# Kernel tuning notes

Measured on AMD Instinct MI355X. Metric: run time of the kernel, lower is better.

Reference implementation:

```python
import jax, jax.numpy as jnp
import numpy as np

N_NODES = 50000
N_EDGES = 800000
IN_CH, HID_CH, OUT_CH = 128, 128, 64


def setup_inputs() -> dict:
    key = jax.random.key(0)
    ks = jax.random.split(key, 8)
    x = jax.random.normal(ks[0], (N_NODES, IN_CH), dtype=jnp.float32)
    edge_index = jax.random.randint(ks[1], (2, N_EDGES), 0, N_NODES, dtype=jnp.int64)
    # PyG SAGEConv params: lin_l (applied to aggregated neighbors, has bias),
    # lin_r (applied to root node, no bias). Stored here as [in, out] matrices.
    s1 = 1.0 / np.sqrt(IN_CH)
    s2 = 1.0 / np.sqrt(HID_CH)
    W1l = jax.random.uniform(ks[2], (IN_CH, HID_CH), jnp.float32, -s1, s1)
    b1 = jnp.zeros((HID_CH,), jnp.float32)
    W1r = jax.random.uniform(ks[3], (IN_CH, HID_CH), jnp.float32, -s1, s1)
    W2l = jax.random.uniform(ks[4], (HID_CH, OUT_CH), jnp.float32, -s2, s2)
    b2 = jnp.zeros((OUT_CH,), jnp.float32)
    W2r = jax.random.uniform(ks[5], (HID_CH, OUT_CH), jnp.float32, -s2, s2)
    return {"x": x, "edge_index": edge_index, "W1l": W1l, "b1": b1,
            "W1r": W1r, "W2l": W2l, "b2": b2, "W2r": W2r}


def _sage_conv(x, src, dst, Wl, b, Wr):
    # mean-aggregate source features onto targets, then linear transform
    msg = x[src]                                        # [E, d] gather
    agg = jax.ops.segment_sum(msg, dst, num_segments=N_NODES)   # [N, d]
    deg = jax.ops.segment_sum(jnp.ones((src.shape[0],), x.dtype), dst,
                              num_segments=N_NODES)     # [N]
    mean = agg / jnp.maximum(deg, 1.0)[:, None]
    return mean @ Wl + b + x @ Wr


def reference(x, edge_index, W1l, b1, W1r, W2l, b2, W2r):
    src, dst = edge_index[0], edge_index[1]
    h = jax.nn.relu(_sage_conv(x, src, dst, W1l, b1, W1r))
    # F.dropout(p=0.3) is identity in eval mode
    return _sage_conv(h, src, dst, W2l, b2, W2r)
```

## Files before the change

kernel.cpp:

```cpp
#include <hip/hip_runtime.h>
#include <hip/hip_bf16.h>


#define TBLOCK 256
#define MAXBUCK 256
#define HGRID 512

typedef __attribute__((ext_vector_type(8))) short short8;
typedef __attribute__((ext_vector_type(4))) float f32x4;

__device__ __forceinline__ float bf2f(ushort u) {
    union { unsigned int i; float f; } v;
    v.i = (unsigned int)u << 16;
    return v.f;
}
__device__ __forceinline__ ushort f2bf(float f) {
    union { float f; unsigned int u; } v;
    v.f = f;
    unsigned int r = v.u + 0x7fffu + ((v.u >> 16) & 1u);
    return (ushort)(r >> 16);
}

__device__ __forceinline__ int block_detect_is64(const int* __restrict__ edges) {
    __shared__ int sbad[4];
    int tid = threadIdx.x;
    int bad = 0;
    for (int i = tid; i < 2048; i += TBLOCK)
        if (edges[2 * i + 1] != 0) bad = 1;
    unsigned long long b = __ballot(bad);
    if ((tid & 63) == 0) sbad[tid >> 6] = (b != 0) ? 1 : 0;
    __syncthreads();
    int flag = (sbad[0] | sbad[1] | sbad[2] | sbad[3]) ? 0 : 1;
    __syncthreads();
    return flag;
}

__device__ __forceinline__ int load_src(const int* e, long long i, int E, int is64) {
    return is64 ? e[2 * i] : e[i];
}
__device__ __forceinline__ int load_dst(const int* e, long long i, int E, int is64) {
    return is64 ? e[2 * (long long)E + 2 * i] : e[(long long)E + i];
}

__device__ __forceinline__ void scan_total(const int* __restrict__ total, int NBUCK,
                                           int* __restrict__ s) {
    int t = threadIdx.x;
    s[t] = (t < NBUCK) ? total[t] : 0;
    __syncthreads();
    for (int off = 1; off < TBLOCK; off <<= 1) {
        int xv = (t >= off) ? s[t - off] : 0;
        __syncthreads();
        s[t] += xv;
        __syncthreads();
    }
}

__global__ __launch_bounds__(TBLOCK) void histprep_k(
    const float* __restrict__ x,
    const float* __restrict__ W1l, const float* __restrict__ W1r,
    const float* __restrict__ W2l, const float* __restrict__ W2r,
    const int* __restrict__ edges, int E, int NBUCK,
    ushort* __restrict__ xb, ushort* __restrict__ wc1, ushort* __restrict__ wc2,
    int* __restrict__ counts, int n8, int nxb) {
    __shared__ int lh[MAXBUCK];
    const int b = blockIdx.x;
    const int t = threadIdx.x;
    if (b < HGRID) {
        const int is64 = block_detect_is64(edges);
        for (int i = t; i < NBUCK; i += TBLOCK) lh[i] = 0;
        __syncthreads();
        const int per = (E + HGRID - 1) / HGRID;
        const int b0 = b * per, b1 = min(E, b0 + per);
        for (int i = b0 + t; i < b1; i += TBLOCK)
            atomicAdd(&lh[load_dst(edges, i, E, is64) >> 8], 1);
        __syncthreads();
        for (int j = t; j < NBUCK; j += TBLOCK)
            counts[j * HGRID + b] = lh[j];
    } else {
        int pb = b - HGRID;
        if (pb < nxb) {
            int i = pb * TBLOCK + t;
            if (i >= n8) return;
            const float4* p = (const float4*)x + (size_t)i * 2;
            float4 a = p[0], bb = p[1];
            short8 o;
            o[0] = f2bf(a.x); o[1] = f2bf(a.y); o[2] = f2bf(a.z); o[3] = f2bf(a.w);
            o[4] = f2bf(bb.x); o[5] = f2bf(bb.y); o[6] = f2bf(bb.z); o[7] = f2bf(bb.w);
            *(short8*)(xb + (size_t)i * 8) = o;
        } else {
            int i = (pb - nxb) * TBLOCK + t;
            if (i < 32768) {
                int j = i & 7;
                int rest = i >> 3;
                int n = rest & 127;
                int k = ((rest >> 7) << 3) | j;
                float w = (k < 128) ? W1l[k * 128 + n] : W1r[(k - 128) * 128 + n];
                wc1[i] = f2bf(w);
            } else if (i < 49152) {
                int i2 = i - 32768;
                int j = i2 & 7;
                int rest = i2 >> 3;
                int n = rest & 127;
                int k = ((rest >> 7) << 3) | j;
                float w = (n < 64) ? W2l[k * 64 + n] : W2r[k * 64 + (n - 64)];
                wc2[i2] = f2bf(w);
            }
        }
    }
}

__global__ __launch_bounds__(TBLOCK) void scanA_k(int* __restrict__ counts,
                                                  int* __restrict__ total) {
    __shared__ int s[TBLOCK];
    const int j = blockIdx.x;
    const int t = threadIdx.x;
    int* row = counts + (size_t)j * HGRID;
    int v0 = row[2 * t];
    int v1 = row[2 * t + 1];
    s[t] = v0 + v1;
    __syncthreads();
    for (int off = 1; off < TBLOCK; off <<= 1) {
        int xv = (t >= off) ? s[t - off] : 0;
        __syncthreads();
        s[t] += xv;
        __syncthreads();
    }
    int excl = (t == 0) ? 0 : s[t - 1];
    row[2 * t] = excl;
    row[2 * t + 1] = excl + v0;
    if (t == TBLOCK - 1) total[j] = s[t];
}

__global__ __launch_bounds__(TBLOCK) void scatroot_k(
    const int* __restrict__ edges, int E,
    const int* __restrict__ counts, const int* __restrict__ total,
    unsigned int* __restrict__ packed, int NBUCK,
    const ushort* __restrict__ xb, const ushort* __restrict__ wc1,
    const float* __restrict__ b1, ushort* __restrict__ hb, int N, int RB) {
    __shared__ __align__(16) ushort sW[128 * 128];
    __shared__ int s[TBLOCK];
    __shared__ int lb[MAXBUCK];
    __shared__ int lh[MAXBUCK];
    const int t = threadIdx.x;

    if ((int)blockIdx.x < RB) {
        const ushort* wroot = wc1 + 16384;
        for (int i = t * 8; i < 128 * 128; i += TBLOCK * 8)
            *(short8*)&sW[i] = *(const short8*)&wroot[i];
        __syncthreads();
        const int wave = t >> 6;
        const int lane = t & 63;
        const int quad = lane >> 4;
        const int l16 = lane & 15;
        const int m0 = (blockIdx.x * 4 + wave) * 32;
        if (m0 >= N) return;
        f32x4 acc[2][8];
#pragma unroll
        for (int tt = 0; tt < 2; tt++)
#pragma unroll
            for (int nt = 0; nt < 8; nt++) acc[tt][nt] = (f32x4){0.f, 0.f, 0.f, 0.f};
        const int k0q = quad * 8;
#pragma unroll
        for (int kb = 0; kb < 128; kb += 32) {
            int k = kb + k0q;
            short8 a[2];
#pragma unroll
            for (int tt = 0; tt < 2; tt++) {
                int m = m0 + tt * 16 + l16;
                if (m > N - 1) m = N - 1;
                a[tt] = *(const short8*)(xb + (size_t)m * 128 + k);
            }
#pragma unroll
            for (int nt = 0; nt < 8; nt++) {
                short8 b = *(const short8*)&sW[((k >> 3) * 128 + nt * 16 + l16) * 8];
                acc[0][nt] = __builtin_amdgcn_mfma_f32_16x16x32_bf16(a[0], b, acc[0][nt], 0, 0, 0);
                acc[1][nt] = __builtin_amdgcn_mfma_f32_16x16x32_bf16(a[1], b, acc[1][nt], 0, 0, 0);
            }
        }
#pragma unroll
        for (int tt = 0; tt < 2; tt++)
#pragma unroll
            for (int r = 0; r < 4; r++) {
                int m = m0 + tt * 16 + quad * 4 + r;
                if (m >= N) continue;
#pragma unroll
                for (int nt = 0; nt < 8; nt++) {
                    int n = nt * 16 + l16;
                    hb[(size_t)m * 128 + n] = f2bf(acc[tt][nt][r] + b1[n]);
                }
            }
    } else {
        const int b = blockIdx.x - RB;
        const int is64 = block_detect_is64(edges);
        scan_total(total, NBUCK, s);
        if (t < NBUCK) {
            int excl = (t == 0) ? 0 : s[t - 1];
            lb[t] = excl + counts[t * HGRID + b];
            lh[t] = 0;
        }
        __syncthreads();
        const int per = (E + HGRID - 1) / HGRID;
        const int b0 = b * per, b1e = min(E, b0 + per);
        for (int i = b0 + t; i < b1e; i += TBLOCK) {
            int sv = load_src(edges, i, E, is64);
            int d = load_dst(edges, i, E, is64);
            int bk = d >> 8;
            int pos = lb[bk] + atomicAdd(&lh[bk], 1);
            packed[pos] = (unsigned int)sv | ((unsigned int)(d & 255) << 24);
        }
    }
}

__global__ __launch_bounds__(TBLOCK) void buildB_k(const unsigned int* __restrict__ packed,
                                                   const int* __restrict__ total,
                                                   int* __restrict__ offs,
                                                   int* __restrict__ degi,
                                                   float* __restrict__ invdeg,
                                                   int* __restrict__ csr, int N, int NBUCK) {
    __shared__ int s[TBLOCK];
    __shared__ int cnt[TBLOCK], scn[TBLOCK], cur[TBLOCK];
    int t = threadIdx.x;
    int bucket = blockIdx.x;
    scan_total(total, NBUCK, s);
    int e0 = (bucket == 0) ? 0 : s[bucket - 1];
    int e1 = s[bucket];
    cnt[t] = 0;
    cur[t] = 0;
    __syncthreads();
    for (int i = e0 + t; i < e1; i += TBLOCK)
        atomicAdd(&cnt[packed[i] >> 24], 1);
    __syncthreads();
    scn[t] = cnt[t];
    __syncthreads();
    for (int off = 1; off < TBLOCK; off <<= 1) {
        int x = (t >= off) ? scn[t - off] : 0;
        __syncthreads();
        scn[t] += x;
        __syncthreads();
    }
    int excl = (t == 0) ? 0 : scn[t - 1];
    int node = bucket * 256 + t;
    if (node < N) {
        offs[node] = e0 + excl;
        degi[node] = cnt[t];
        invdeg[node] = 1.0f / fmaxf((float)cnt[t], 1.0f);
    }
    __syncthreads();
    cnt[t] = excl;
    __syncthreads();
    for (int i = e0 + t; i < e1; i += TBLOCK) {
        unsigned int p = packed[i];
        int nl = p >> 24;
        int pos = e0 + cnt[nl] + atomicAdd(&cur[nl], 1);
        csr[pos] = (int)(p & 0xFFFFFFu);
    }
}

template <int C, bool ACCUM>
__global__ __launch_bounds__(TBLOCK) void gatherb_k(const ushort* __restrict__ feat,
                                                    const int* __restrict__ csr,
                                                    const int* __restrict__ offs,
                                                    const int* __restrict__ degi,
                                                    const float* __restrict__ invdeg,
                                                    ushort* __restrict__ outB,
                                                    float* __restrict__ outF, int N) {
    constexpr int G = C / 8;
    constexpr int NPB = TBLOCK / G;
    int n = blockIdx.x * NPB + threadIdx.x / G;
    if (n >= N) return;
    int lane = threadIdx.x % G;
    int c = lane * 8;
    int s0 = offs[n];
    int d = degi[n];
    float acc[8] = {0.f, 0.f, 0.f, 0.f, 0.f, 0.f, 0.f, 0.f};
    for (int base = 0; base < d; base += G) {
        int rem = d - base;
        int my = (lane < rem) ? csr[s0 + base + lane] : 0;
        if (rem >= G) {
#pragma unroll
            for (int j = 0; j < G; j++) {
                int s = __shfl(my, j, G);
                short8 v = *(const short8*)(feat + (size_t)s * C + c);
#pragma unroll
                for (int q = 0; q < 8; q++) acc[q] += bf2f((ushort)v[q]);
            }
        } else {
            for (int j = 0; j < rem; j++) {
                int s = __shfl(my, j, G);
                short8 v = *(const short8*)(feat + (size_t)s * C + c);
#pragma unroll
                for (int q = 0; q < 8; q++) acc[q] += bf2f((ushort)v[q]);
            }
        }
    }
    float sc = invdeg[n];
    if (ACCUM) {
        float* o = outF + (size_t)n * C + c;
        float4 p0 = *(float4*)o;
        float4 p1 = *(float4*)(o + 4);
        p0.x += sc * acc[0]; p0.y += sc * acc[1]; p0.z += sc * acc[2]; p0.w += sc * acc[3];
        p1.x += sc * acc[4]; p1.y += sc * acc[5]; p1.z += sc * acc[6]; p1.w += sc * acc[7];
        *(float4*)o = p0;
        *(float4*)(o + 4) = p1;
    } else {
        short8 o;
#pragma unroll
        for (int q = 0; q < 8; q++) o[q] = f2bf(sc * acc[q]);
        *(short8*)(outB + (size_t)n * C + c) = o;
    }
}

__global__ __launch_bounds__(TBLOCK) void gemm1b_k(const ushort* __restrict__ agg1b,
                                                   const ushort* __restrict__ wc1,
                                                   ushort* __restrict__ hb, int N) {
    __shared__ __align__(16) ushort sW[128 * 128];
    for (int i = threadIdx.x * 8; i < 128 * 128; i += TBLOCK * 8)
        *(short8*)&sW[i] = *(const short8*)&wc1[i];
    __syncthreads();

    const int wave = threadIdx.x >> 6;
    const int lane = threadIdx.x & 63;
    const int quad = lane >> 4;
    const int l16 = lane & 15;
    const int m0 = (blockIdx.x * 4 + wave) * 32;
    if (m0 >= N) return;

    f32x4 acc[2][8];
#pragma unroll
    for (int t = 0; t < 2; t++)
#pragma unroll
        for (int nt = 0; nt < 8; nt++) acc[t][nt] = (f32x4){0.f, 0.f, 0.f, 0.f};

    const int k0q = quad * 8;
#pragma unroll
    for (int kb = 0; kb < 128; kb += 32) {
        int k = kb + k0q;
        short8 a[2];
#pragma unroll
        for (int t = 0; t < 2; t++) {
            int m = m0 + t * 16 + l16;
            if (m > N - 1) m = N - 1;
            a[t] = *(const short8*)(agg1b + (size_t)m * 128 + k);
        }
#pragma unroll
        for (int nt = 0; nt < 8; nt++) {
            short8 b = *(const short8*)&sW[((k >> 3) * 128 + nt * 16 + l16) * 8];
            acc[0][nt] = __builtin_amdgcn_mfma_f32_16x16x32_bf16(a[0], b, acc[0][nt], 0, 0, 0);
            acc[1][nt] = __builtin_amdgcn_mfma_f32_16x16x32_bf16(a[1], b, acc[1][nt], 0, 0, 0);
        }
    }

#pragma unroll
    for (int t = 0; t < 2; t++) {
#pragma unroll
        for (int r = 0; r < 4; r++) {
            int m = m0 + t * 16 + quad * 4 + r;
            if (m >= N) continue;
#pragma unroll
            for (int nt = 0; nt < 8; nt++) {
                int n = nt * 16 + l16;
                float v = acc[t][nt][r] + bf2f(hb[(size_t)m * 128 + n]);
                hb[(size_t)m * 128 + n] = f2bf(fmaxf(v, 0.f));
            }
        }
    }
}

__global__ __launch_bounds__(TBLOCK) void gemm2_k(const ushort* __restrict__ A0,
                                                  const ushort* __restrict__ wc,
                                                  const float* __restrict__ bias,
                                                  ushort* __restrict__ outB,
                                                  float* __restrict__ outF, int N) {
    constexpr int KTOT = 128;
    __shared__ __align__(16) ushort sW[KTOT * 128];
    for (int i = threadIdx.x * 8; i < KTOT * 128; i += TBLOCK * 8)
        *(short8*)&sW[i] = *(const short8*)&wc[i];
    __syncthreads();

    const int wave = threadIdx.x >> 6;
    const int lane = threadIdx.x & 63;
    const int quad = lane >> 4;
    const int l16 = lane & 15;
    const int m0 = (blockIdx.x * 4 + wave) * 32;
    if (m0 >= N) return;

    f32x4 acc[2][8];
#pragma unroll
    for (int t = 0; t < 2; t++)
#pragma unroll
        for (int nt = 0; nt < 8; nt++) acc[t][nt] = (f32x4){0.f, 0.f, 0.f, 0.f};

    const int k0q = quad * 8;
#pragma unroll
    for (int kb = 0; kb < KTOT; kb += 32) {
        int k = kb + k0q;
        short8 a[2];
#pragma unroll
        for (int t = 0; t < 2; t++) {
            int m = m0 + t * 16 + l16;
            if (m > N - 1) m = N - 1;
            a[t] = *(const short8*)(A0 + (size_t)m * 128 + k);
        }
#pragma unroll
        for (int nt = 0; nt < 8; nt++) {
            short8 b = *(const short8*)&sW[((k >> 3) * 128 + nt * 16 + l16) * 8];
            acc[0][nt] = __builtin_amdgcn_mfma_f32_16x16x32_bf16(a[0], b, acc[0][nt], 0, 0, 0);
            acc[1][nt] = __builtin_amdgcn_mfma_f32_16x16x32_bf16(a[1], b, acc[1][nt], 0, 0, 0);
        }
    }

#pragma unroll
    for (int t = 0; t < 2; t++) {
#pragma unroll
        for (int r = 0; r < 4; r++) {
            int m = m0 + t * 16 + quad * 4 + r;
            if (m >= N) continue;
#pragma unroll
            for (int nt = 0; nt < 8; nt++) {
                int n = nt * 16 + l16;
                float v = acc[t][nt][r];
                if (n < 64) outB[(size_t)m * 64 + n] = f2bf(v);
                else outF[(size_t)m * 64 + (n - 64)] = v + bias[n - 64];
            }
        }
    }
}

extern "C" void kernel_launch(void* const* d_in, const int* in_sizes, int n_in,
                              void* d_out, int out_size, void* d_ws, size_t ws_size,
                              hipStream_t stream) {
    const float* x = (const float*)d_in[0];
    const int* edges = (const int*)d_in[1];
    const float* W1l = (const float*)d_in[2];
    const float* b1 = (const float*)d_in[3];
    const float* W1r = (const float*)d_in[4];
    const float* W2l = (const float*)d_in[5];
    const float* b2 = (const float*)d_in[6];
    const float* W2r = (const float*)d_in[7];
    float* out = (float*)d_out;

    const int N = in_sizes[0] / 128;
    const int E = in_sizes[1] / 2;
    const int Na = (N + 63) & ~63;
    const int NBUCK = (N + 255) >> 8;
    const int n8 = N * 128 / 8;
    const int nxb = (n8 + TBLOCK - 1) / TBLOCK;
    const int RB = (N + 127) / 128;

    char* WS = (char*)d_ws;
    size_t off = 0;
    auto alloc = [&](size_t bytes) {
        void* p = WS + off;
        off = (off + bytes + 255) & ~(size_t)255;
        return p;
    };
    int* counts = (int*)alloc((size_t)MAXBUCK * HGRID * 4);
    int* total = (int*)alloc((size_t)MAXBUCK * 4);
    int* offs = (int*)alloc((size_t)Na * 4);
    int* degi = (int*)alloc((size_t)Na * 4);
    float* invdeg = (float*)alloc((size_t)Na * 4);
    unsigned int* packed = (unsigned int*)alloc((size_t)E * 4);
    int* csr = (int*)alloc((size_t)E * 4);
    ushort* xb = (ushort*)alloc((size_t)N * 128 * 2);
    ushort* agg1b = (ushort*)alloc((size_t)N * 128 * 2);
    ushort* hb = (ushort*)alloc((size_t)N * 128 * 2);
    ushort* t2b = (ushort*)alloc((size_t)N * 64 * 2);
    ushort* wc1 = (ushort*)alloc(32768 * 2);
    ushort* wc2 = (ushort*)alloc(16384 * 2);

    histprep_k<<<HGRID + nxb + 192, TBLOCK, 0, stream>>>(
        x, W1l, W1r, W2l, W2r, edges, E, NBUCK, xb, wc1, wc2, counts, n8, nxb);
    scanA_k<<<NBUCK, TBLOCK, 0, stream>>>(counts, total);
    scatroot_k<<<RB + HGRID, TBLOCK, 0, stream>>>(
        edges, E, counts, total, packed, NBUCK, xb, wc1, b1, hb, N, RB);
    buildB_k<<<NBUCK, TBLOCK, 0, stream>>>(packed, total, offs, degi, invdeg, csr, N, NBUCK);

    gatherb_k<128, false><<<(N + 15) / 16, TBLOCK, 0, stream>>>(
        xb, csr, offs, degi, invdeg, agg1b, nullptr, N);
    gemm1b_k<<<(N + 127) / 128, TBLOCK, 0, stream>>>(agg1b, wc1, hb, N);

    gemm2_k<<<(N + 127) / 128, TBLOCK, 0, stream>>>(
        hb, wc2, b2, t2b, out, N);
    gatherb_k<64, true><<<(N + 31) / 32, TBLOCK, 0, stream>>>(
        t2b, csr, offs, degi, invdeg, nullptr, out, N);
}
```

Measured before the change: 194.2 us.

## Fuse layer-1 and layer-2 GEMMs, keeping hidden activations in LDS

Merges the two GEMM kernels into one. The ReLU'd hidden tile is staged in padded shared memory, then multiplied by the second weight matrix in the same block. This removes the global write and re-read of the hidden activations and one kernel launch. In exchange, LDS use per block roughly doubles (weights plus the hidden tile), which may lower occupancy, and an extra weight reload and barriers are added.

```diff
diff --git a/kernel.cpp b/kernel.cpp
--- a/kernel.cpp
+++ b/kernel.cpp
@@ -5,6 +5,7 @@
 #define TBLOCK 256
 #define MAXBUCK 256
 #define HGRID 512
+#define HPAD 136
 
 typedef __attribute__((ext_vector_type(8))) short short8;
 typedef __attribute__((ext_vector_type(4))) float f32x4;
@@ -310,37 +311,41 @@
     }
 }
 
-__global__ __launch_bounds__(TBLOCK) void gemm1b_k(const ushort* __restrict__ agg1b,
+__global__ __launch_bounds__(TBLOCK) void gemm12_k(const ushort* __restrict__ agg1b,
                                                    const ushort* __restrict__ wc1,
-                                                   ushort* __restrict__ hb, int N) {
+                                                   const ushort* __restrict__ wc2,
+                                                   const ushort* __restrict__ hbB,
+                                                   const float* __restrict__ b2,
+                                                   ushort* __restrict__ t2b,
+                                                   float* __restrict__ outF, int N) {
     __shared__ __align__(16) ushort sW[128 * 128];
-    for (int i = threadIdx.x * 8; i < 128 * 128; i += TBLOCK * 8)
-        *(short8*)&sW[i] = *(const short8*)&wc1[i];
-    __syncthreads();
-
-    const int wave = threadIdx.x >> 6;
-    const int lane = threadIdx.x & 63;
+    __shared__ __align__(16) ushort hbt[128 * HPAD];
+    const int t = threadIdx.x;
+    const int wave = t >> 6;
+    const int lane = t & 63;
     const int quad = lane >> 4;
     const int l16 = lane & 15;
-    const int m0 = (blockIdx.x * 4 + wave) * 32;
-    if (m0 >= N) return;
+    const int m0 = blockIdx.x * 128 + wave * 32;
+    const int k0q = quad * 8;
+
+    for (int i = t * 8; i < 128 * 128; i += TBLOCK * 8)
+        *(short8*)&sW[i] = *(const short8*)&wc1[i];
+    __syncthreads();
 
     f32x4 acc[2][8];
 #pragma unroll
-    for (int t = 0; t < 2; t++)
-#pragma unroll
-        for (int nt = 0; nt < 8; nt++) acc[t][nt] = (f32x4){0.f, 0.f, 0.f, 0.f};
-
-    const int k0q = quad * 8;
+    for (int tt = 0; tt < 2; tt++)
+#pragma unroll
+        for (int nt = 0; nt < 8; nt++) acc[tt][nt] = (f32x4){0.f, 0.f, 0.f, 0.f};
 #pragma unroll
     for (int kb = 0; kb < 128; kb += 32) {
         int k = kb + k0q;
         short8 a[2];
 #pragma unroll
-        for (int t = 0; t < 2; t++) {
-            int m = m0 + t * 16 + l16;
+        for (int tt = 0; tt < 2; tt++) {
+            int m = m0 + tt * 16 + l16;
             if (m > N - 1) m = N - 1;
-            a[t] = *(const short8*)(agg1b + (size_t)m * 128 + k);
+            a[tt] = *(const short8*)(agg1b + (size_t)m * 128 + k);
         }
 #pragma unroll
         for (int nt = 0; nt < 8; nt++) {
@@ -351,79 +356,59 @@
     }
 
 #pragma unroll
-    for (int t = 0; t < 2; t++) {
+    for (int tt = 0; tt < 2; tt++)
 #pragma unroll
         for (int r = 0; r < 4; r++) {
-            int m = m0 + t * 16 + quad * 4 + r;
-            if (m >= N) continue;
+            int ml = wave * 32 + tt * 16 + quad * 4 + r;
+            int m = m0 + tt * 16 + quad * 4 + r;
+            int mc = (m < N) ? m : N - 1;
 #pragma unroll
             for (int nt = 0; nt < 8; nt++) {
                 int n = nt * 16 + l16;
-                float v = acc[t][nt][r] + bf2f(hb[(size_t)m * 128 + n]);
-                hb[(size_t)m * 128 + n] = f2bf(fmaxf(v, 0.f));
-            }
-        }
-    }
-}
-
-__global__ __launch_bounds__(TBLOCK) void gemm2_k(const ushort* __restrict__ A0,
-                                                  const ushort* __restrict__ wc,
-                                                  const float* __restrict__ bias,
-                                                  ushort* __restrict__ outB,
-                                                  float* __restrict__ outF, int N) {
-    constexpr int KTOT = 128;
-    __shared__ __align__(16) ushort sW[KTOT * 128];
-    for (int i = threadIdx.x * 8; i < KTOT * 128; i += TBLOCK * 8)
-        *(short8*)&sW[i] = *(const short8*)&wc[i];
-    __syncthreads();
-
-    const int wave = threadIdx.x >> 6;
-    const int lane = threadIdx.x & 63;
-    const int quad = lane >> 4;
-    const int l16 = lane & 15;
-    const int m0 = (blockIdx.x * 4 + wave) * 32;
-    if (m0 >= N) return;
-
-    f32x4 acc[2][8];
-#pragma unroll
-    for (int t = 0; t < 2; t++)
-#pragma unroll
-        for (int nt = 0; nt < 8; nt++) acc[t][nt] = (f32x4){0.f, 0.f, 0.f, 0.f};
-
-    const int k0q = quad * 8;
-#pragma unroll
-    for (int kb = 0; kb < KTOT; kb += 32) {
+                float v = acc[tt][nt][r] + bf2f(hbB[(size_t)mc * 128 + n]);
+                hbt[ml * HPAD + n] = f2bf(fmaxf(v, 0.f));
+            }
+        }
+    __syncthreads();
+
+    for (int i = t * 8; i < 128 * 128; i += TBLOCK * 8)
+        *(short8*)&sW[i] = *(const short8*)&wc2[i];
+    __syncthreads();
+
+    f32x4 acc2[2][8];
+#pragma unroll
+    for (int tt = 0; tt < 2; tt++)
+#pragma unroll
+        for (int nt = 0; nt < 8; nt++) acc2[tt][nt] = (f32x4){0.f, 0.f, 0.f, 0.f};
+#pragma unroll
+    for (int kb = 0; kb < 128; kb += 32) {
         int k = kb + k0q;
         short8 a[2];
 #pragma unroll
-        for (int t = 0; t < 2; t++) {
-            int m = m0 + t * 16 + l16;
-            if (m > N - 1) m = N - 1;
-            a[t] = *(const short8*)(A0 + (size_t)m * 128 + k);
-        }
+        for (int tt = 0; tt < 2; tt++)
+            a[tt] = *(const short8*)&hbt[(wave * 32 + tt * 16 + l16) * HPAD + k];
 #pragma unroll
         for (int nt = 0; nt < 8; nt++) {
             short8 b = *(const short8*)&sW[((k >> 3) * 128 + nt * 16 + l16) * 8];
-            acc[0][nt] = __builtin_amdgcn_mfma_f32_16x16x32_bf16(a[0], b, acc[0][nt], 0, 0, 0);
-            acc[1][nt] = __builtin_amdgcn_mfma_f32_16x16x32_bf16(a[1], b, acc[1][nt], 0, 0, 0);
-        }
-    }
-
-#pragma unroll
-    for (int t = 0; t < 2; t++) {
+            acc2[0][nt] = __builtin_amdgcn_mfma_f32_16x16x32_bf16(a[0], b, acc2[0][nt], 0, 0, 0);
+            acc2[1][nt] = __builtin_amdgcn_mfma_f32_16x16x32_bf16(a[1], b, acc2[1][nt], 0, 0, 0);
+        }
+    }
+
+#pragma unroll
+    for (int tt = 0; tt < 2; tt++)
 #pragma unroll
         for (int r = 0; r < 4; r++) {
-            int m = m0 + t * 16 + quad * 4 + r;
+            int m = m0 + tt * 16 + quad * 4 + r;
             if (m >= N) continue;
 #pragma unroll
             for (int nt = 0; nt < 8; nt++) {
                 int n = nt * 16 + l16;
-                float v = acc[t][nt][r];
-                if (n < 64) outB[(size_t)m * 64 + n] = f2bf(v);
-                else outF[(size_t)m * 64 + (n - 64)] = v + bias[n - 64];
-            }
-        }
-    }
+                float v = acc2[tt][nt][r];
+                if (n < 64) t2b[(size_t)m * 64 + n] = f2bf(v);
+                else outF[(size_t)m * 64 + (n - 64)] = v + b2[n - 64];
+            }
+        }
 }
 
 extern "C" void kernel_launch(void* const* d_in, const int* in_sizes, int n_in,
@@ -477,10 +462,8 @@
 
     gatherb_k<128, false><<<(N + 15) / 16, TBLOCK, 0, stream>>>(
         xb, csr, offs, degi, invdeg, agg1b, nullptr, N);
-    gemm1b_k<<<(N + 127) / 128, TBLOCK, 0, stream>>>(agg1b, wc1, hb, N);
-
-    gemm2_k<<<(N + 127) / 128, TBLOCK, 0, stream>>>(
-        hb, wc2, b2, t2b, out, N);
+    gemm12_k<<<(N + 127) / 128, TBLOCK, 0, stream>>>(
+        agg1b, wc1, wc2, hb, b2, t2b, out, N);
     gatherb_k<64, true><<<(N + 31) / 32, TBLOCK, 0, stream>>>(
         t2b, csr, offs, degi, invdeg, nullptr, out, N);
 }
```

New measurement: 187.8 us, median of 2. 3.3% less time.
